# Kernel tuning notes

Hardware: AMD Instinct MI355X
Metric: run time of the kernel (lower is better)

The kernel has to match this reference:

```python
import jax, jax.numpy as jnp
import numpy as np

B, S, D, H = 4, 2048, 1024, 16
DK = D // H


def setup_inputs() -> dict:
    key = jax.random.key(0)
    k1, k2, k3, k4 = jax.random.split(key, 4)
    x = jax.random.normal(k1, (B, S, D), dtype=jnp.float32)
    # torch nn.Linear stores weight as [out, in]; y = x @ W.T + b
    w_qkv = jax.random.normal(k2, (3 * D, D), dtype=jnp.float32) * (1.0 / np.sqrt(D))
    b_qkv = jax.random.normal(k3, (3 * D,), dtype=jnp.float32) * 0.02
    w_o = jax.random.normal(k4, (D, D), dtype=jnp.float32) * (1.0 / np.sqrt(D))
    # causal mask: True where attention is disallowed (masked_fill semantics)
    mask = jnp.triu(jnp.ones((S, S), dtype=bool), k=1)[None, None]  # [1,1,S,S]
    return {"encodings_for_qkv": x, "mask": mask, "w_qkv": w_qkv, "b_qkv": b_qkv, "w_o": w_o}


def reference(encodings_for_qkv, mask, w_qkv, b_qkv, w_o):
    x = encodings_for_qkv
    qkv = x @ w_qkv.T + b_qkv                      # [B,S,3D]
    q, k, v = jnp.split(qkv, 3, axis=-1)           # each [B,S,D]

    def heads(t):
        return t.reshape(B, S, H, DK).transpose(0, 2, 1, 3)  # [B,H,S,DK]

    q, k, v = heads(q), heads(k), heads(v)
    scale = 1.0 / np.sqrt(DK).astype(np.float32)
    sims = jnp.einsum('bhqd,bhkd->bhqk', q, k) * scale       # [B,H,S,S]
    sims = jnp.where(mask, jnp.float32(-1e9), sims)
    attn = jax.nn.softmax(sims, axis=-1)
    out = jnp.einsum('bhqk,bhkd->bhqd', attn, v)             # [B,H,S,DK]
    out = out.transpose(0, 2, 1, 3).reshape(B, S, D)
    return out @ w_o.T
```

## Files before the change

kernel.cpp:

```cpp
#include <hip/hip_runtime.h>
#include <hip/hip_bf16.h>

typedef __attribute__((ext_vector_type(8))) __bf16 bf16x8;
typedef __attribute__((ext_vector_type(4))) __bf16 bf16x4;
typedef __attribute__((ext_vector_type(4))) float f32x4;

constexpr int B = 4, S = 2048, D = 1024, H = 16, DK = 64;

#define GLOAD16(gp, lp)                                                              \
  __builtin_amdgcn_global_load_lds((const __attribute__((address_space(1))) void*)(gp), \
                                   (__attribute__((address_space(3))) void*)(lp), 16, 0, 0)

__global__ __launch_bounds__(256) void convert_bf16(const float* __restrict__ X,
                                                    const float* __restrict__ Wqkv,
                                                    const float* __restrict__ Wo,
                                                    __bf16* __restrict__ Xb,
                                                    __bf16* __restrict__ Wqkvb,
                                                    __bf16* __restrict__ Wob) {
  const int NX = B * S * D;
  const int NW = 3 * D * D;
  const int NO = D * D;
  const int total8 = (NX + NW + NO) / 8;
  for (int i = blockIdx.x * blockDim.x + threadIdx.x; i < total8;
       i += gridDim.x * blockDim.x) {
    const int e = i * 8;
    const float* src;
    __bf16* dst;
    int off;
    if (e < NX) {
      src = X; dst = Xb; off = e;
    } else if (e < NX + NW) {
      src = Wqkv; dst = Wqkvb; off = e - NX;
    } else {
      src = Wo; dst = Wob; off = e - NX - NW;
    }
    float4 a = *reinterpret_cast<const float4*>(src + off);
    float4 b = *reinterpret_cast<const float4*>(src + off + 4);
    bf16x8 v = {(__bf16)a.x, (__bf16)a.y, (__bf16)a.z, (__bf16)a.w,
                (__bf16)b.x, (__bf16)b.y, (__bf16)b.z, (__bf16)b.w};
    *reinterpret_cast<bf16x8*>(dst + off) = v;
  }
}

__global__ __launch_bounds__(256) void qkv_gemm(const __bf16* __restrict__ Xb,
                                                const __bf16* __restrict__ Wb,
                                                const float* __restrict__ bias,
                                                __bf16* __restrict__ Qb,
                                                __bf16* __restrict__ Kb,
                                                __bf16* __restrict__ VTb) {
  __shared__ __bf16 As[2][128 * 64];
  __shared__ __bf16 Bs[2][128 * 64];
  const int tid = threadIdx.x;
  const int lane = tid & 63;
  const int w = tid >> 6;
  const int wr = w >> 1, wc = w & 1;
  const int lr = lane & 15, lb = lane >> 4;
  const int m0 = blockIdx.x * 128, n0 = blockIdx.y * 128;

  int srow[4], sgcol[4];
#pragma unroll
  for (int rnd = 0; rnd < 4; ++rnd) {
    const int i = rnd * 256 + tid;
    srow[rnd] = i >> 3;
    sgcol[rnd] = ((i & 7) ^ (srow[rnd] & 7)) << 3;
  }

  f32x4 acc[4][4];
#pragma unroll
  for (int i = 0; i < 4; ++i)
#pragma unroll
    for (int j = 0; j < 4; ++j) acc[i][j] = f32x4{0.f, 0.f, 0.f, 0.f};

#pragma unroll
  for (int rnd = 0; rnd < 4; ++rnd) {
    GLOAD16(&Xb[(size_t)(m0 + srow[rnd]) * D + sgcol[rnd]],
            (char*)&As[0][0] + rnd * 4096 + w * 1024);
    GLOAD16(&Wb[(size_t)(n0 + srow[rnd]) * D + sgcol[rnd]],
            (char*)&Bs[0][0] + rnd * 4096 + w * 1024);
  }
  __syncthreads();

  int cur = 0;
  for (int k0 = 0; k0 < D; k0 += 64) {
    if (k0 + 64 < D) {
#pragma unroll
      for (int rnd = 0; rnd < 4; ++rnd) {
        GLOAD16(&Xb[(size_t)(m0 + srow[rnd]) * D + k0 + 64 + sgcol[rnd]],
                (char*)&As[cur ^ 1][0] + rnd * 4096 + w * 1024);
        GLOAD16(&Wb[(size_t)(n0 + srow[rnd]) * D + k0 + 64 + sgcol[rnd]],
                (char*)&Bs[cur ^ 1][0] + rnd * 4096 + w * 1024);
      }
    }

    bf16x8 af[4][2], bfr[4][2];
#pragma unroll
    for (int m = 0; m < 4; ++m) {
      const int row = wr * 64 + m * 16 + lr;
#pragma unroll
      for (int ks = 0; ks < 2; ++ks)
        af[m][ks] = *reinterpret_cast<const bf16x8*>(
            (const char*)&As[cur][0] + row * 128 + (((ks * 32 + lb * 8) << 1) ^ ((row & 7) << 4)));
    }
#pragma unroll
    for (int n = 0; n < 4; ++n) {
      const int row = wc * 64 + n * 16 + lr;
#pragma unroll
      for (int ks = 0; ks < 2; ++ks)
        bfr[n][ks] = *reinterpret_cast<const bf16x8*>(
            (const char*)&Bs[cur][0] + row * 128 + (((ks * 32 + lb * 8) << 1) ^ ((row & 7) << 4)));
    }
#pragma unroll
    for (int m = 0; m < 4; ++m)
#pragma unroll
      for (int n = 0; n < 4; ++n) {
        acc[m][n] = __builtin_amdgcn_mfma_f32_16x16x32_bf16(af[m][0], bfr[n][0], acc[m][n], 0, 0, 0);
        acc[m][n] = __builtin_amdgcn_mfma_f32_16x16x32_bf16(af[m][1], bfr[n][1], acc[m][n], 0, 0, 0);
      }
    __syncthreads();
    cur ^= 1;
  }

  const int seg = n0 >> 10;
  if (seg == 2) {
#pragma unroll
    for (int m = 0; m < 4; ++m) {
      const int tb = m0 + wr * 64 + m * 16 + lb * 4;
      const int bb2 = tb >> 11;
      const int s = tb & 2047;
#pragma unroll
      for (int n = 0; n < 4; ++n) {
        const int c = n0 + wc * 64 + n * 16 + lr;
        const int cc = c & 1023;
        const int h = cc >> 6, dk = cc & 63;
        const float bv = bias[c];
        bf16x4 pv;
#pragma unroll
        for (int r = 0; r < 4; ++r) pv[r] = (__bf16)(acc[m][n][r] + bv);
        *reinterpret_cast<bf16x4*>(
            &VTb[(((size_t)bb2 * H + h) * DK + dk) * S + s]) = pv;
      }
    }
  } else {
#pragma unroll
    for (int m = 0; m < 4; ++m)
#pragma unroll
      for (int n = 0; n < 4; ++n) {
        const int c = n0 + wc * 64 + n * 16 + lr;
        const int cc = c & 1023;
        const int h = cc >> 6, dk = cc & 63;
        const float bv = bias[c];
#pragma unroll
        for (int r = 0; r < 4; ++r) {
          const int t = m0 + wr * 64 + m * 16 + lb * 4 + r;
          const int bb2 = t >> 11;
          const int s = t & 2047;
          const float v = acc[m][n][r] + bv;
          const size_t bh = (size_t)bb2 * H + h;
          if (seg == 0)
            Qb[(bh * S + s) * DK + dk] = (__bf16)(v * 0.180336893f);
          else
            Kb[(bh * S + s) * DK + dk] = (__bf16)v;
        }
      }
  }
}

__global__ __launch_bounds__(512, 4) void attn_fwd(const __bf16* __restrict__ Qb,
                                                   const __bf16* __restrict__ Kb,
                                                   const __bf16* __restrict__ VTb,
                                                   __bf16* __restrict__ AO) {
  __shared__ __bf16 Kl[64 * 64];
  __shared__ __bf16 Vl[64 * 64];
  __shared__ __bf16 Ps[8][16][72];
  const int tid = threadIdx.x;
  const int lane = tid & 63;
  const int w = tid >> 6;
  const int lr = lane & 15, lb = lane >> 4;

  const int flat = blockIdx.x;
  const int xcd = flat & 7;
  const int idx = flat >> 3;
  const int hg = idx & 7;
  const int pr = idx >> 3;
  const int bh = hg * 8 + xcd;
  const int bb = bh >> 4, h = bh & 15;

  const __bf16* Q = Qb + (size_t)bh * S * DK;
  const __bf16* K = Kb + (size_t)bh * S * DK;
  const __bf16* VT = VTb + (size_t)bh * DK * S;

  const int srow = tid >> 3;
  const int sc8 = (tid & 7) * 8;
  const int sbyte = srow * 128 + sc8 * 2;
  const int sswz = (srow & 7) << 4;
  const int rsw = (lr & 7) << 4;

  bf16x8 ones;
#pragma unroll
  for (int i = 0; i < 8; ++i) ones[i] = (__bf16)1.0f;

  for (int pass = 0; pass < 2; ++pass) {
    const int qt = pass ? (15 - pr) : pr;
    const int q0w = qt * 128 + w * 16;
    const int nt = 2 * qt + 2;
    const int ntw = 2 * qt + 1 + (w >> 2);

    bf16x8 qf[2];
#pragma unroll
    for (int d = 0; d < 2; ++d)
      qf[d] = *reinterpret_cast<const bf16x8*>(
          &Q[(size_t)(q0w + lr) * DK + d * 32 + lb * 8]);

    {
      bf16x8 k0 = *reinterpret_cast<const bf16x8*>(K + (size_t)srow * DK + sc8);
      bf16x8 v0 = *reinterpret_cast<const bf16x8*>(VT + (size_t)srow * S + sc8);
      *reinterpret_cast<bf16x8*>((char*)&Kl[0] + (sbyte ^ sswz)) = k0;
      *reinterpret_cast<bf16x8*>((char*)&Vl[0] + (sbyte ^ sswz)) = v0;
    }
    __syncthreads();

    f32x4 o[4], lsum;
#pragma unroll
    for (int n = 0; n < 4; ++n) o[n] = f32x4{0.f, 0.f, 0.f, 0.f};
    lsum = f32x4{0.f, 0.f, 0.f, 0.f};
    float mrun = -1e30f;

    for (int t = 0; t < nt; ++t) {
      const int kv0 = t * 64;
      const bool have_next = (t + 1 < nt);
      bf16x8 gk0, gv0;
      if (have_next) {
        gk0 = *reinterpret_cast<const bf16x8*>(K + ((size_t)(kv0 + 64) + srow) * DK + sc8);
        gv0 = *reinterpret_cast<const bf16x8*>(VT + (size_t)srow * S + (kv0 + 64) + sc8);
      }

      if (t < ntw) {
        const char* kbase = (const char*)&Kl[0];
        const char* vbase = (const char*)&Vl[0];
        bf16x8 kf[4][2];
#pragma unroll
        for (int kc = 0; kc < 4; ++kc)
#pragma unroll
          for (int d = 0; d < 2; ++d)
            kf[kc][d] = *reinterpret_cast<const bf16x8*>(
                kbase + (kc * 16 + lr) * 128 + ((d * 64 + lb * 16) ^ rsw));

        f32x4 st[4];
        __builtin_amdgcn_s_setprio(1);
#pragma unroll
        for (int kc = 0; kc < 4; ++kc) {
          f32x4 z = f32x4{0.f, 0.f, 0.f, 0.f};
          z = __builtin_amdgcn_mfma_f32_16x16x32_bf16(kf[kc][0], qf[0], z, 0, 0, 0);
          z = __builtin_amdgcn_mfma_f32_16x16x32_bf16(kf[kc][1], qf[1], z, 0, 0, 0);
          st[kc] = z;
        }
        __builtin_amdgcn_s_setprio(0);

        if (t == ntw - 1) {
          const int qg = q0w + lr;
#pragma unroll
          for (int kc = 0; kc < 4; ++kc)
#pragma unroll
            for (int r = 0; r < 4; ++r) {
              const int kg = kv0 + kc * 16 + 4 * lb + r;
              if (kg > qg) st[kc][r] = -1e30f;
            }
        }

        float a0 = fmaxf(fmaxf(st[0][0], st[0][1]), fmaxf(st[0][2], st[0][3]));
        float a1 = fmaxf(fmaxf(st[1][0], st[1][1]), fmaxf(st[1][2], st[1][3]));
        float a2 = fmaxf(fmaxf(st[2][0], st[2][1]), fmaxf(st[2][2], st[2][3]));
        float a3 = fmaxf(fmaxf(st[3][0], st[3][1]), fmaxf(st[3][2], st[3][3]));
        float mx = fmaxf(fmaxf(a0, a1), fmaxf(a2, a3));
        mx = fmaxf(mx, __shfl_xor(mx, 16, 64));
        mx = fmaxf(mx, __shfl_xor(mx, 32, 64));

        if (__any(mx > mrun + 11.f)) {
          const float nm = fmaxf(mrun, mx);
          const float alpha = exp2f(mrun - nm);
          mrun = nm;
#pragma unroll
          for (int r = 0; r < 4; ++r) {
            const float ao = __shfl(alpha, 4 * lb + r, 64);
#pragma unroll
            for (int n = 0; n < 4; ++n) o[n][r] *= ao;
            lsum[r] *= ao;
          }
        }

#pragma unroll
        for (int kc = 0; kc < 4; ++kc) {
          bf16x4 pk;
#pragma unroll
          for (int r = 0; r < 4; ++r) pk[r] = (__bf16)exp2f(st[kc][r] - mrun);
          *reinterpret_cast<bf16x4*>(&Ps[w][lr][kc * 16 + 4 * lb]) = pk;
        }

        asm volatile("s_waitcnt lgkmcnt(0)" ::: "memory");
        __builtin_amdgcn_sched_barrier(0);

        bf16x8 pa[2];
#pragma unroll
        for (int ks = 0; ks < 2; ++ks)
          pa[ks] = *reinterpret_cast<const bf16x8*>(&Ps[w][lr][ks * 32 + lb * 8]);
        bf16x8 vf[4][2];
#pragma unroll
        for (int n = 0; n < 4; ++n)
#pragma unroll
          for (int ks = 0; ks < 2; ++ks)
            vf[n][ks] = *reinterpret_cast<const bf16x8*>(
                vbase + (n * 16 + lr) * 128 + ((ks * 64 + lb * 16) ^ rsw));

        __builtin_amdgcn_s_setprio(1);
#pragma unroll
        for (int n = 0; n < 4; ++n) {
          o[n] = __builtin_amdgcn_mfma_f32_16x16x32_bf16(pa[0], vf[n][0], o[n], 0, 0, 0);
          o[n] = __builtin_amdgcn_mfma_f32_16x16x32_bf16(pa[1], vf[n][1], o[n], 0, 0, 0);
        }
        lsum = __builtin_amdgcn_mfma_f32_16x16x32_bf16(pa[0], ones, lsum, 0, 0, 0);
        lsum = __builtin_amdgcn_mfma_f32_16x16x32_bf16(pa[1], ones, lsum, 0, 0, 0);
        __builtin_amdgcn_s_setprio(0);
      }

      __syncthreads();
      if (have_next) {
        *reinterpret_cast<bf16x8*>((char*)&Kl[0] + (sbyte ^ sswz)) = gk0;
        *reinterpret_cast<bf16x8*>((char*)&Vl[0] + (sbyte ^ sswz)) = gv0;
      }
      __syncthreads();
    }

#pragma unroll
    for (int r = 0; r < 4; ++r) {
      const float inv = 1.f / lsum[r];
      const int q = q0w + 4 * lb + r;
#pragma unroll
      for (int n = 0; n < 4; ++n)
        AO[((size_t)(bb * S + q)) * D + h * DK + n * 16 + lr] = (__bf16)(o[n][r] * inv);
    }
  }
}

__global__ __launch_bounds__(256) void out_gemm(const __bf16* __restrict__ AOp,
                                                const __bf16* __restrict__ Wb,
                                                float* __restrict__ Out) {
  __shared__ __bf16 As[2][128 * 64];
  __shared__ __bf16 Bs[2][128 * 64];
  const int tid = threadIdx.x;
  const int lane = tid & 63;
  const int w = tid >> 6;
  const int wr = w >> 1, wc = w & 1;
  const int lr = lane & 15, lb = lane >> 4;
  const int m0 = blockIdx.x * 128, n0 = blockIdx.y * 128;

  int srow[4], sgcol[4];
#pragma unroll
  for (int rnd = 0; rnd < 4; ++rnd) {
    const int i = rnd * 256 + tid;
    srow[rnd] = i >> 3;
    sgcol[rnd] = ((i & 7) ^ (srow[rnd] & 7)) << 3;
  }

  f32x4 acc[4][4];
#pragma unroll
  for (int i = 0; i < 4; ++i)
#pragma unroll
    for (int j = 0; j < 4; ++j) acc[i][j] = f32x4{0.f, 0.f, 0.f, 0.f};

#pragma unroll
  for (int rnd = 0; rnd < 4; ++rnd) {
    GLOAD16(&AOp[(size_t)(m0 + srow[rnd]) * D + sgcol[rnd]],
            (char*)&As[0][0] + rnd * 4096 + w * 1024);
    GLOAD16(&Wb[(size_t)(n0 + srow[rnd]) * D + sgcol[rnd]],
            (char*)&Bs[0][0] + rnd * 4096 + w * 1024);
  }
  __syncthreads();

  int cur = 0;
  for (int k0 = 0; k0 < D; k0 += 64) {
    if (k0 + 64 < D) {
#pragma unroll
      for (int rnd = 0; rnd < 4; ++rnd) {
        GLOAD16(&AOp[(size_t)(m0 + srow[rnd]) * D + k0 + 64 + sgcol[rnd]],
                (char*)&As[cur ^ 1][0] + rnd * 4096 + w * 1024);
        GLOAD16(&Wb[(size_t)(n0 + srow[rnd]) * D + k0 + 64 + sgcol[rnd]],
                (char*)&Bs[cur ^ 1][0] + rnd * 4096 + w * 1024);
      }
    }

    bf16x8 af[4][2], bfr[4][2];
#pragma unroll
    for (int m = 0; m < 4; ++m) {
      const int row = wr * 64 + m * 16 + lr;
#pragma unroll
      for (int ks = 0; ks < 2; ++ks)
        af[m][ks] = *reinterpret_cast<const bf16x8*>(
            (const char*)&As[cur][0] + row * 128 + (((ks * 32 + lb * 8) << 1) ^ ((row & 7) << 4)));
    }
#pragma unroll
    for (int n = 0; n < 4; ++n) {
      const int row = wc * 64 + n * 16 + lr;
#pragma unroll
      for (int ks = 0; ks < 2; ++ks)
        bfr[n][ks] = *reinterpret_cast<const bf16x8*>(
            (const char*)&Bs[cur][0] + row * 128 + (((ks * 32 + lb * 8) << 1) ^ ((row & 7) << 4)));
    }
#pragma unroll
    for (int m = 0; m < 4; ++m)
#pragma unroll
      for (int n = 0; n < 4; ++n) {
        acc[m][n] = __builtin_amdgcn_mfma_f32_16x16x32_bf16(af[m][0], bfr[n][0], acc[m][n], 0, 0, 0);
        acc[m][n] = __builtin_amdgcn_mfma_f32_16x16x32_bf16(af[m][1], bfr[n][1], acc[m][n], 0, 0, 0);
      }
    __syncthreads();
    cur ^= 1;
  }

#pragma unroll
  for (int m = 0; m < 4; ++m)
#pragma unroll
    for (int n = 0; n < 4; ++n)
#pragma unroll
      for (int r = 0; r < 4; ++r)
        Out[(size_t)(m0 + wr * 64 + m * 16 + lb * 4 + r) * D + n0 + wc * 64 + n * 16 + lr] =
            acc[m][n][r];
}

extern "C" void kernel_launch(void* const* d_in, const int* in_sizes, int n_in,
                              void* d_out, int out_size, void* d_ws, size_t ws_size,
                              hipStream_t stream) {
  (void)in_sizes; (void)n_in; (void)out_size; (void)ws_size;
  const float* x = (const float*)d_in[0];
  const float* w_qkv = (const float*)d_in[2];
  const float* b_qkv = (const float*)d_in[3];
  const float* w_o = (const float*)d_in[4];
  float* out = (float*)d_out;

  const size_t qkv_elems = (size_t)B * H * S * DK;
  __bf16* Qb = (__bf16*)d_ws;
  __bf16* Kb = Qb + qkv_elems;
  __bf16* VTb = Kb + qkv_elems;
  __bf16* AO = VTb + qkv_elems;
  __bf16* Xb = AO + qkv_elems;
  __bf16* Wqkvb = Xb + (size_t)B * S * D;
  __bf16* Wob = Wqkvb + (size_t)3 * D * D;

  convert_bf16<<<2048, 256, 0, stream>>>(x, w_qkv, w_o, Xb, Wqkvb, Wob);
  qkv_gemm<<<dim3(64, 24), 256, 0, stream>>>(Xb, Wqkvb, b_qkv, Qb, Kb, VTb);
  attn_fwd<<<dim3(8 * (B * H)), 512, 0, stream>>>(Qb, Kb, VTb, AO);
  out_gemm<<<dim3(64, 8), 256, 0, stream>>>(AO, Wob, out);
}
```

Measured before the change: 166.7 us.

## Widen attention KV tile from 64 to 128 keys per iteration

The attention kernel now stages 128 keys of K and V per loop iteration instead of 64, which halves the number of tile iterations and the __syncthreads barriers per pass. Each wave processes eight score chunks and four PV k-steps per tile, with a matching 128-wide swizzled V layout. Because the q tile is 128 rows, the per-wave skip of the final half tile is dropped, so some waves compute fully masked scores on the diagonal tile. The change also raises LDS use and register pressure under the 512-thread, 4-block launch bounds, which risks spills or lower occupancy.

```diff
diff --git a/kernel.cpp b/kernel.cpp
--- a/kernel.cpp
+++ b/kernel.cpp
@@ -169,9 +169,9 @@
                                                    const __bf16* __restrict__ Kb,
                                                    const __bf16* __restrict__ VTb,
                                                    __bf16* __restrict__ AO) {
-  __shared__ __bf16 Kl[64 * 64];
-  __shared__ __bf16 Vl[64 * 64];
-  __shared__ __bf16 Ps[8][16][72];
+  __shared__ __bf16 Kl[128 * 64];
+  __shared__ __bf16 Vl[64 * 128];
+  __shared__ __bf16 Ps[8][16][136];
   const int tid = threadIdx.x;
   const int lane = tid & 63;
   const int w = tid >> 6;
@@ -189,10 +189,12 @@
   const __bf16* K = Kb + (size_t)bh * S * DK;
   const __bf16* VT = VTb + (size_t)bh * DK * S;
 
-  const int srow = tid >> 3;
-  const int sc8 = (tid & 7) * 8;
-  const int sbyte = srow * 128 + sc8 * 2;
-  const int sswz = (srow & 7) << 4;
+  const int krow = tid >> 3;
+  const int c8 = (tid & 7) * 8;
+  const int kswz = (krow & 7) << 4;
+  const int kb0 = krow * 128 + ((c8 * 2) ^ kswz);
+  const int vb0 = krow * 256 + ((c8 * 2) ^ kswz);
+  const int vb1 = krow * 256 + (((c8 * 2) + 128) ^ kswz);
   const int rsw = (lr & 7) << 4;
 
   bf16x8 ones;
@@ -202,8 +204,7 @@
   for (int pass = 0; pass < 2; ++pass) {
     const int qt = pass ? (15 - pr) : pr;
     const int q0w = qt * 128 + w * 16;
-    const int nt = 2 * qt + 2;
-    const int ntw = 2 * qt + 1 + (w >> 2);
+    const int nt = qt + 1;
 
     bf16x8 qf[2];
 #pragma unroll
@@ -212,10 +213,14 @@
           &Q[(size_t)(q0w + lr) * DK + d * 32 + lb * 8]);
 
     {
-      bf16x8 k0 = *reinterpret_cast<const bf16x8*>(K + (size_t)srow * DK + sc8);
-      bf16x8 v0 = *reinterpret_cast<const bf16x8*>(VT + (size_t)srow * S + sc8);
-      *reinterpret_cast<bf16x8*>((char*)&Kl[0] + (sbyte ^ sswz)) = k0;
-      *reinterpret_cast<bf16x8*>((char*)&Vl[0] + (sbyte ^ sswz)) = v0;
+      bf16x8 k0 = *reinterpret_cast<const bf16x8*>(K + (size_t)krow * DK + c8);
+      bf16x8 k1 = *reinterpret_cast<const bf16x8*>(K + (size_t)(64 + krow) * DK + c8);
+      bf16x8 v0 = *reinterpret_cast<const bf16x8*>(VT + (size_t)krow * S + c8);
+      bf16x8 v1 = *reinterpret_cast<const bf16x8*>(VT + (size_t)krow * S + 64 + c8);
+      *reinterpret_cast<bf16x8*>((char*)&Kl[0] + kb0) = k0;
+      *reinterpret_cast<bf16x8*>((char*)&Kl[0] + kb0 + 8192) = k1;
+      *reinterpret_cast<bf16x8*>((char*)&Vl[0] + vb0) = v0;
+      *reinterpret_cast<bf16x8*>((char*)&Vl[0] + vb1) = v1;
     }
     __syncthreads();
 
@@ -226,106 +231,109 @@
     float mrun = -1e30f;
 
     for (int t = 0; t < nt; ++t) {
-      const int kv0 = t * 64;
+      const int kv0 = t * 128;
       const bool have_next = (t + 1 < nt);
-      bf16x8 gk0, gv0;
+      bf16x8 gk0, gk1, gv0, gv1;
       if (have_next) {
-        gk0 = *reinterpret_cast<const bf16x8*>(K + ((size_t)(kv0 + 64) + srow) * DK + sc8);
-        gv0 = *reinterpret_cast<const bf16x8*>(VT + (size_t)srow * S + (kv0 + 64) + sc8);
-      }
-
-      if (t < ntw) {
-        const char* kbase = (const char*)&Kl[0];
-        const char* vbase = (const char*)&Vl[0];
-        bf16x8 kf[4][2];
-#pragma unroll
-        for (int kc = 0; kc < 4; ++kc)
-#pragma unroll
-          for (int d = 0; d < 2; ++d)
-            kf[kc][d] = *reinterpret_cast<const bf16x8*>(
-                kbase + (kc * 16 + lr) * 128 + ((d * 64 + lb * 16) ^ rsw));
-
-        f32x4 st[4];
-        __builtin_amdgcn_s_setprio(1);
-#pragma unroll
-        for (int kc = 0; kc < 4; ++kc) {
-          f32x4 z = f32x4{0.f, 0.f, 0.f, 0.f};
-          z = __builtin_amdgcn_mfma_f32_16x16x32_bf16(kf[kc][0], qf[0], z, 0, 0, 0);
-          z = __builtin_amdgcn_mfma_f32_16x16x32_bf16(kf[kc][1], qf[1], z, 0, 0, 0);
-          st[kc] = z;
+        gk0 = *reinterpret_cast<const bf16x8*>(K + (size_t)(kv0 + 128 + krow) * DK + c8);
+        gk1 = *reinterpret_cast<const bf16x8*>(K + (size_t)(kv0 + 192 + krow) * DK + c8);
+        gv0 = *reinterpret_cast<const bf16x8*>(VT + (size_t)krow * S + kv0 + 128 + c8);
+        gv1 = *reinterpret_cast<const bf16x8*>(VT + (size_t)krow * S + kv0 + 192 + c8);
+      }
+
+      f32x4 st[8];
+      __builtin_amdgcn_s_setprio(1);
+#pragma unroll
+      for (int kc = 0; kc < 8; ++kc) {
+        const int row = kc * 16 + lr;
+        bf16x8 kf0 = *reinterpret_cast<const bf16x8*>(
+            (const char*)&Kl[0] + row * 128 + ((lb * 16) ^ rsw));
+        bf16x8 kf1 = *reinterpret_cast<const bf16x8*>(
+            (const char*)&Kl[0] + row * 128 + ((64 + lb * 16) ^ rsw));
+        f32x4 z = f32x4{0.f, 0.f, 0.f, 0.f};
+        z = __builtin_amdgcn_mfma_f32_16x16x32_bf16(kf0, qf[0], z, 0, 0, 0);
+        z = __builtin_amdgcn_mfma_f32_16x16x32_bf16(kf1, qf[1], z, 0, 0, 0);
+        st[kc] = z;
+      }
+      __builtin_amdgcn_s_setprio(0);
+
+      if (t == nt - 1) {
+        const int qg = q0w + lr;
+#pragma unroll
+        for (int kc = 0; kc < 8; ++kc)
+#pragma unroll
+          for (int r = 0; r < 4; ++r) {
+            const int kg = kv0 + kc * 16 + 4 * lb + r;
+            if (kg > qg) st[kc][r] = -1e30f;
+          }
+      }
+
+      float a0 = fmaxf(fmaxf(st[0][0], st[0][1]), fmaxf(st[0][2], st[0][3]));
+      float a1 = fmaxf(fmaxf(st[1][0], st[1][1]), fmaxf(st[1][2], st[1][3]));
+      float a2 = fmaxf(fmaxf(st[2][0], st[2][1]), fmaxf(st[2][2], st[2][3]));
+      float a3 = fmaxf(fmaxf(st[3][0], st[3][1]), fmaxf(st[3][2], st[3][3]));
+      float a4 = fmaxf(fmaxf(st[4][0], st[4][1]), fmaxf(st[4][2], st[4][3]));
+      float a5 = fmaxf(fmaxf(st[5][0], st[5][1]), fmaxf(st[5][2], st[5][3]));
+      float a6 = fmaxf(fmaxf(st[6][0], st[6][1]), fmaxf(st[6][2], st[6][3]));
+      float a7 = fmaxf(fmaxf(st[7][0], st[7][1]), fmaxf(st[7][2], st[7][3]));
+      float mx = fmaxf(fmaxf(fmaxf(a0, a1), fmaxf(a2, a3)),
+                       fmaxf(fmaxf(a4, a5), fmaxf(a6, a7)));
+      mx = fmaxf(mx, __shfl_xor(mx, 16, 64));
+      mx = fmaxf(mx, __shfl_xor(mx, 32, 64));
+
+      if (__any(mx > mrun + 11.f)) {
+        const float nm = fmaxf(mrun, mx);
+        const float alpha = exp2f(mrun - nm);
+        mrun = nm;
+#pragma unroll
+        for (int r = 0; r < 4; ++r) {
+          const float ao = __shfl(alpha, 4 * lb + r, 64);
+#pragma unroll
+          for (int n = 0; n < 4; ++n) o[n][r] *= ao;
+          lsum[r] *= ao;
         }
-        __builtin_amdgcn_s_setprio(0);
-
-        if (t == ntw - 1) {
-          const int qg = q0w + lr;
-#pragma unroll
-          for (int kc = 0; kc < 4; ++kc)
-#pragma unroll
-            for (int r = 0; r < 4; ++r) {
-              const int kg = kv0 + kc * 16 + 4 * lb + r;
-              if (kg > qg) st[kc][r] = -1e30f;
-            }
+      }
+
+#pragma unroll
+      for (int kc = 0; kc < 8; ++kc) {
+        bf16x4 pk;
+#pragma unroll
+        for (int r = 0; r < 4; ++r) pk[r] = (__bf16)exp2f(st[kc][r] - mrun);
+        *reinterpret_cast<bf16x4*>(&Ps[w][lr][kc * 16 + 4 * lb]) = pk;
+      }
+
+      asm volatile("s_waitcnt lgkmcnt(0)" ::: "memory");
+      __builtin_amdgcn_sched_barrier(0);
+
+      bf16x4* dummy;  (void)dummy;
+      bf16x8 pa[4];
+#pragma unroll
+      for (int ks = 0; ks < 4; ++ks)
+        pa[ks] = *reinterpret_cast<const bf16x8*>(&Ps[w][lr][ks * 32 + lb * 8]);
+
+      __builtin_amdgcn_s_setprio(1);
+#pragma unroll
+      for (int n = 0; n < 4; ++n) {
+        const int row = n * 16 + lr;
+        const char* rb = (const char*)&Vl[0] + row * 256;
+#pragma unroll
+        for (int ks = 0; ks < 4; ++ks) {
+          bf16x8 vf = *reinterpret_cast<const bf16x8*>(
+              rb + ((ks * 64 + lb * 16) ^ rsw));
+          o[n] = __builtin_amdgcn_mfma_f32_16x16x32_bf16(pa[ks], vf, o[n], 0, 0, 0);
         }
-
-        float a0 = fmaxf(fmaxf(st[0][0], st[0][1]), fmaxf(st[0][2], st[0][3]));
-        float a1 = fmaxf(fmaxf(st[1][0], st[1][1]), fmaxf(st[1][2], st[1][3]));
-        float a2 = fmaxf(fmaxf(st[2][0], st[2][1]), fmaxf(st[2][2], st[2][3]));
-        float a3 = fmaxf(fmaxf(st[3][0], st[3][1]), fmaxf(st[3][2], st[3][3]));
-        float mx = fmaxf(fmaxf(a0, a1), fmaxf(a2, a3));
-        mx = fmaxf(mx, __shfl_xor(mx, 16, 64));
-        mx = fmaxf(mx, __shfl_xor(mx, 32, 64));
-
-        if (__any(mx > mrun + 11.f)) {
-          const float nm = fmaxf(mrun, mx);
-          const float alpha = exp2f(mrun - nm);
-          mrun = nm;
-#pragma unroll
-          for (int r = 0; r < 4; ++r) {
-            const float ao = __shfl(alpha, 4 * lb + r, 64);
-#pragma unroll
-            for (int n = 0; n < 4; ++n) o[n][r] *= ao;
-            lsum[r] *= ao;
-          }
-        }
-
-#pragma unroll
-        for (int kc = 0; kc < 4; ++kc) {
-          bf16x4 pk;
-#pragma unroll
-          for (int r = 0; r < 4; ++r) pk[r] = (__bf16)exp2f(st[kc][r] - mrun);
-          *reinterpret_cast<bf16x4*>(&Ps[w][lr][kc * 16 + 4 * lb]) = pk;
-        }
-
-        asm volatile("s_waitcnt lgkmcnt(0)" ::: "memory");
-        __builtin_amdgcn_sched_barrier(0);
-
-        bf16x8 pa[2];
-#pragma unroll
-        for (int ks = 0; ks < 2; ++ks)
-          pa[ks] = *reinterpret_cast<const bf16x8*>(&Ps[w][lr][ks * 32 + lb * 8]);
-        bf16x8 vf[4][2];
-#pragma unroll
-        for (int n = 0; n < 4; ++n)
-#pragma unroll
-          for (int ks = 0; ks < 2; ++ks)
-            vf[n][ks] = *reinterpret_cast<const bf16x8*>(
-                vbase + (n * 16 + lr) * 128 + ((ks * 64 + lb * 16) ^ rsw));
-
-        __builtin_amdgcn_s_setprio(1);
-#pragma unroll
-        for (int n = 0; n < 4; ++n) {
-          o[n] = __builtin_amdgcn_mfma_f32_16x16x32_bf16(pa[0], vf[n][0], o[n], 0, 0, 0);
-          o[n] = __builtin_amdgcn_mfma_f32_16x16x32_bf16(pa[1], vf[n][1], o[n], 0, 0, 0);
-        }
-        lsum = __builtin_amdgcn_mfma_f32_16x16x32_bf16(pa[0], ones, lsum, 0, 0, 0);
-        lsum = __builtin_amdgcn_mfma_f32_16x16x32_bf16(pa[1], ones, lsum, 0, 0, 0);
-        __builtin_amdgcn_s_setprio(0);
-      }
+      }
+#pragma unroll
+      for (int ks = 0; ks < 4; ++ks)
+        lsum = __builtin_amdgcn_mfma_f32_16x16x32_bf16(pa[ks], ones, lsum, 0, 0, 0);
+      __builtin_amdgcn_s_setprio(0);
 
       __syncthreads();
       if (have_next) {
-        *reinterpret_cast<bf16x8*>((char*)&Kl[0] + (sbyte ^ sswz)) = gk0;
-        *reinterpret_cast<bf16x8*>((char*)&Vl[0] + (sbyte ^ sswz)) = gv0;
+        *reinterpret_cast<bf16x8*>((char*)&Kl[0] + kb0) = gk0;
+        *reinterpret_cast<bf16x8*>((char*)&Kl[0] + kb0 + 8192) = gk1;
+        *reinterpret_cast<bf16x8*>((char*)&Vl[0] + vb0) = gv0;
+        *reinterpret_cast<bf16x8*>((char*)&Vl[0] + vb1) = gv1;
       }
       __syncthreads();
     }
```

Result: no change. 169.0 us (+1.4%).
